# Performance work log

Measured on AMD Instinct MI355X. Metric: run time of the kernel, lower is better.

The kernel has to match this reference:

```python
import jax, jax.numpy as jnp
import numpy as np

N_NODES = 100000
N_EDGES = 1600000
IN_DIM = 128
HID = 128


def setup_inputs() -> dict:
    key = jax.random.key(0)
    ks = jax.random.split(key, 8)
    x = jax.random.normal(ks[0], (N_NODES, IN_DIM), dtype=jnp.float32)
    edge_index = jax.random.randint(ks[1], (2, N_EDGES), 0, N_NODES, dtype=jnp.int32)
    s = 1.0 / np.sqrt(IN_DIM)
    # layer 1: in_dim -> hidden; layer 2: hidden -> hidden
    Wl1 = jax.random.uniform(ks[2], (IN_DIM, HID), jnp.float32, -s, s)
    bl1 = jnp.zeros((HID,), jnp.float32)
    Wr1 = jax.random.uniform(ks[3], (IN_DIM, HID), jnp.float32, -s, s)
    s2 = 1.0 / np.sqrt(HID)
    Wl2 = jax.random.uniform(ks[4], (HID, HID), jnp.float32, -s2, s2)
    bl2 = jnp.zeros((HID,), jnp.float32)
    Wr2 = jax.random.uniform(ks[5], (HID, HID), jnp.float32, -s2, s2)
    return {"x": x, "edge_index": edge_index, "Wl1": Wl1, "bl1": bl1, "Wr1": Wr1,
            "Wl2": Wl2, "bl2": bl2, "Wr2": Wr2}


def _sage_conv(h, src, dst, Wl, bl, Wr, n_nodes):
    # mean aggregation of neighbor (source) features at destination nodes
    msg = h[src]                                               # [E, D] gather
    agg = jax.ops.segment_sum(msg, dst, num_segments=n_nodes)  # [N, D]
    deg = jax.ops.segment_sum(jnp.ones((src.shape[0],), h.dtype), dst,
                              num_segments=n_nodes)            # [N]
    agg = agg / jnp.maximum(deg, 1.0)[:, None]
    # PyG SAGEConv: lin_l(aggregated) + lin_r(root); lin_r has no bias
    return agg @ Wl + bl + h @ Wr


def reference(x, edge_index, Wl1, bl1, Wr1, Wl2, bl2, Wr2):
    src, dst = edge_index[0], edge_index[1]
    n = x.shape[0]
    h = jax.nn.relu(_sage_conv(x, src, dst, Wl1, bl1, Wr1, n))
    # dropout is identity in eval mode
    h = jax.nn.relu(_sage_conv(h, src, dst, Wl2, bl2, Wr2, n))
    return h
```

## Files before the change

kernel.cpp:

```cpp
#include <hip/hip_runtime.h>
#include <stdint.h>

#define DIM 128

typedef __attribute__((ext_vector_type(8))) short short8;
typedef __attribute__((ext_vector_type(4))) float floatx4;

__device__ __forceinline__ unsigned short f2bf(float f){
  union { float f; unsigned int i; } c; c.f = f;
  unsigned int u = c.i;
  return (unsigned short)((u + 0x7fffu + ((u >> 16) & 1u)) >> 16);
}
__device__ __forceinline__ float up_lo(unsigned int v){ return __uint_as_float(v << 16); }
__device__ __forceinline__ float up_hi(unsigned int v){ return __uint_as_float(v & 0xffff0000u); }


__global__ __launch_bounds__(256) void k_cast(const float* __restrict__ in,
    unsigned short* __restrict__ out, int n4){
  int i = blockIdx.x * 256 + threadIdx.x;
  int stride = gridDim.x * 256;
  for (; i < n4; i += stride){
    float4 v = ((const float4*)in)[i];
    ushort4 o;
    o.x = f2bf(v.x); o.y = f2bf(v.y); o.z = f2bf(v.z); o.w = f2bf(v.w);
    ((ushort4*)out)[i] = o;
  }
}


__global__ __launch_bounds__(256) void k_hist256(const int* __restrict__ dst, int E,
    int* __restrict__ bktCnt){
  __shared__ int h[256];
  h[threadIdx.x] = 0;
  __syncthreads();
  int i = blockIdx.x * 256 + threadIdx.x;
  int stride = gridDim.x * 256;
  for (; i < E; i += stride) atomicAdd(&h[dst[i] >> 9], 1);
  __syncthreads();
  int v = h[threadIdx.x];
  if (v) atomicAdd(&bktCnt[threadIdx.x], v);
}

__global__ __launch_bounds__(256) void k_scanB(const int* __restrict__ bktCnt,
    int* __restrict__ bktBase, int NB){
  __shared__ int sd[256];
  int t = threadIdx.x;
  int v = (t < NB) ? bktCnt[t] : 0;
  sd[t] = v;
  __syncthreads();
  #pragma unroll
  for (int off = 1; off < 256; off <<= 1){
    int x = (t >= off) ? sd[t - off] : 0;
    __syncthreads();
    sd[t] += x;
    __syncthreads();
  }
  bktBase[t] = sd[t] - v;
}


__global__ __launch_bounds__(256) void k_hist(const int* __restrict__ dst, int E,
                                              int* __restrict__ deg){
  int e = blockIdx.x * 256 + threadIdx.x;
  if (e < E) atomicAdd(&deg[dst[e]], 1);
}

__global__ __launch_bounds__(256) void k_scan1(const int* __restrict__ deg, int N,
    int* __restrict__ out, int* __restrict__ bsum){
  __shared__ int sd[256];
  int t = threadIdx.x;
  int base = blockIdx.x * 1024 + t * 4;
  int v0=0, v1=0, v2=0, v3=0;
  if (base + 3 < N) { int4 q = *(const int4*)(deg + base); v0=q.x; v1=q.y; v2=q.z; v3=q.w; }
  else {
    if (base + 0 < N) v0 = deg[base + 0];
    if (base + 1 < N) v1 = deg[base + 1];
    if (base + 2 < N) v2 = deg[base + 2];
  }
  int s = v0 + v1 + v2 + v3;
  sd[t] = s;
  __syncthreads();
  #pragma unroll
  for (int off = 1; off < 256; off <<= 1){
    int x = (t >= off) ? sd[t - off] : 0;
    __syncthreads();
    sd[t] += x;
    __syncthreads();
  }
  int inc = sd[t];
  int exc = inc - s;
  if (base + 0 < N) out[base + 0] = exc;
  if (base + 1 < N) out[base + 1] = exc + v0;
  if (base + 2 < N) out[base + 2] = exc + v0 + v1;
  if (base + 3 < N) out[base + 3] = exc + v0 + v1 + v2;
  if (t == 255) bsum[blockIdx.x] = inc;
}

__global__ __launch_bounds__(128) void k_scan2(int* __restrict__ bsum, int nb){
  __shared__ int sd[128];
  int t = threadIdx.x;
  int v = (t < nb) ? bsum[t] : 0;
  sd[t] = v;
  __syncthreads();
  #pragma unroll
  for (int off = 1; off < 128; off <<= 1){
    int x = (t >= off) ? sd[t - off] : 0;
    __syncthreads();
    sd[t] += x;
    __syncthreads();
  }
  if (t < nb) bsum[t] = sd[t] - v;
}

__global__ __launch_bounds__(256) void k_scan3(int* __restrict__ rowptr,
    const int* __restrict__ bsum, int N, int E, int* __restrict__ cursor){
  int i = blockIdx.x * 256 + threadIdx.x;
  if (i < N){
    int v = rowptr[i] + bsum[i >> 10];
    rowptr[i] = v;
    cursor[i] = v;
  }
  if (i == 0) rowptr[N] = E;
}

__global__ __launch_bounds__(256) void k_fill(const int* __restrict__ src,
    const int* __restrict__ dst, int E, int* __restrict__ cursor, int* __restrict__ col){
  int e = blockIdx.x * 256 + threadIdx.x;
  if (e < E){
    int d = dst[e];
    int pos = atomicAdd(&cursor[d], 1);
    col[pos] = src[e];
  }
}


__global__ __launch_bounds__(256) void k_bin(const int* __restrict__ src,
    const int* __restrict__ dst, int E,
    const int* __restrict__ bucketBase, int* __restrict__ cursor,
    int2* __restrict__ binned, int NB){
  __shared__ int2 buf[4096];
  __shared__ unsigned char bidArr[4096];
  __shared__ int cnt[256], startA[256], gstart[256], gbase[256];
  int t = threadIdx.x;
  cnt[t] = 0;
  if (t < NB) gbase[t] = bucketBase[t];
  __syncthreads();
  int base = blockIdx.x * 4096;
  int s_[16], d_[16], r_[16];
  #pragma unroll
  for (int i = 0; i < 16; ++i){
    int e = base + i * 256 + t;
    bool v = (e < E);
    s_[i] = v ? src[e] : 0;
    d_[i] = v ? dst[e] : -1;
    r_[i] = v ? atomicAdd(&cnt[d_[i] >> 9], 1) : 0;
  }
  __syncthreads();
  int v = cnt[t];
  startA[t] = v;
  __syncthreads();
  #pragma unroll
  for (int off = 1; off < 256; off <<= 1){
    int y = (t >= off) ? startA[t - off] : 0;
    __syncthreads();
    startA[t] += y;
    __syncthreads();
  }
  int incl = startA[t];
  __syncthreads();
  startA[t] = incl - v;
  __syncthreads();
  #pragma unroll
  for (int i = 0; i < 16; ++i){
    if (d_[i] >= 0){
      int b = d_[i] >> 9;
      int slot = startA[b] + r_[i];
      buf[slot] = make_int2(s_[i], d_[i]);
      bidArr[slot] = (unsigned char)b;
    }
  }
  if (cnt[t] > 0) gstart[t] = atomicAdd(&cursor[t], cnt[t]);
  __syncthreads();
  int total = startA[255] + cnt[255];
  for (int j = t; j < total; j += 256){
    int b = bidArr[j];
    binned[gbase[b] + gstart[b] + (j - startA[b])] = buf[j];
  }
}


__global__ __launch_bounds__(256) void k_csr2(const int2* __restrict__ binned,
    const int* __restrict__ bktBase, int N, int* __restrict__ rowptr,
    int* __restrict__ col){
  __shared__ int cnt[512], excl[512], cur[512];
  __shared__ int sd[256];
  int b = blockIdx.x;
  int node0 = b << 9;
  int nNodes = min(512, N - node0);
  int t = threadIdx.x;
  cnt[t] = 0; cnt[t + 256] = 0;
  __syncthreads();
  int lo = bktBase[b], hi = bktBase[b + 1];
  for (int e = lo + t; e < hi; e += 256)
    atomicAdd(&cnt[binned[e].y - node0], 1);
  __syncthreads();
  int c0 = cnt[2 * t], c1 = cnt[2 * t + 1];
  int ps = c0 + c1;
  sd[t] = ps;
  __syncthreads();
  #pragma unroll
  for (int off = 1; off < 256; off <<= 1){
    int x = (t >= off) ? sd[t - off] : 0;
    __syncthreads();
    sd[t] += x;
    __syncthreads();
  }
  int pexcl = sd[t] - ps;
  excl[2 * t] = pexcl;
  excl[2 * t + 1] = pexcl + c0;
  cur[2 * t] = 0; cur[2 * t + 1] = 0;
  __syncthreads();
  for (int j = t; j < nNodes; j += 256) rowptr[node0 + j] = lo + excl[j];
  if (t == 0) rowptr[node0 + nNodes] = hi;
  for (int e = lo + t; e < hi; e += 256){
    int2 pr = binned[e];
    int dl = pr.y - node0;
    int loc = atomicAdd(&cur[dl], 1);
    col[lo + excl[dl] + loc] = pr.x;
  }
}


__device__ __forceinline__ void acc8(float* a, uint4 u){
  a[0] += up_lo(u.x); a[1] += up_hi(u.x);
  a[2] += up_lo(u.y); a[3] += up_hi(u.y);
  a[4] += up_lo(u.z); a[5] += up_hi(u.z);
  a[6] += up_lo(u.w); a[7] += up_hi(u.w);
}

__global__ __launch_bounds__(256) void k_agg_bf(const unsigned short* __restrict__ feat,
    const int* __restrict__ rowptr, const int* __restrict__ col,
    unsigned short* __restrict__ out, int N){
  int wid = (blockIdx.x * 256 + threadIdx.x) >> 6;
  if (wid >= N) return;
  int lane = threadIdx.x & 63;
  int q = lane >> 4, s = lane & 15;
  int beg = rowptr[wid], end = rowptr[wid + 1];
  float a[8];
  #pragma unroll
  for (int i = 0; i < 8; ++i) a[i] = 0.f;
  int e = beg;
  for (; e + 16 <= end; e += 16){
    int n0 = col[e + q], n1 = col[e + 4 + q], n2 = col[e + 8 + q], n3 = col[e + 12 + q];
    uint4 u0 = ((const uint4*)(feat + (size_t)n0 * DIM))[s];
    uint4 u1 = ((const uint4*)(feat + (size_t)n1 * DIM))[s];
    uint4 u2 = ((const uint4*)(feat + (size_t)n2 * DIM))[s];
    uint4 u3 = ((const uint4*)(feat + (size_t)n3 * DIM))[s];
    acc8(a, u0); acc8(a, u1); acc8(a, u2); acc8(a, u3);
  }
  for (; e < end; e += 4){
    bool valid = (e + q) < end;
    int idx = valid ? (e + q) : beg;
    int nb = col[idx];
    uint4 u = ((const uint4*)(feat + (size_t)nb * DIM))[s];
    if (valid) acc8(a, u);
  }
  #pragma unroll
  for (int i = 0; i < 8; ++i){
    a[i] += __shfl_xor(a[i], 16, 64);
    a[i] += __shfl_xor(a[i], 32, 64);
  }
  if (q == 0){
    int d = end - beg;
    float r = 1.0f / (float)(d > 1 ? d : 1);
    uint4 o;
    o.x = (unsigned int)f2bf(a[0] * r) | ((unsigned int)f2bf(a[1] * r) << 16);
    o.y = (unsigned int)f2bf(a[2] * r) | ((unsigned int)f2bf(a[3] * r) << 16);
    o.z = (unsigned int)f2bf(a[4] * r) | ((unsigned int)f2bf(a[5] * r) << 16);
    o.w = (unsigned int)f2bf(a[6] * r) | ((unsigned int)f2bf(a[7] * r) << 16);
    ((uint4*)(out + (size_t)wid * DIM))[s] = o;
  }
}


__global__ __launch_bounds__(256) void k_agg_f32(const float* __restrict__ feat,
    const int* __restrict__ rowptr, const int* __restrict__ col,
    unsigned short* __restrict__ out, int N){
  int wid = (blockIdx.x * 256 + threadIdx.x) >> 6;
  if (wid >= N) return;
  int lane = threadIdx.x & 63;
  int beg = rowptr[wid], end = rowptr[wid + 1];
  float a0 = 0.f, a1 = 0.f;
  int off = lane * 2;
  int e = beg;
  for (; e + 4 <= end; e += 4){
    int s0 = col[e], s1 = col[e+1], s2 = col[e+2], s3 = col[e+3];
    float2 v0 = *(const float2*)(feat + (size_t)s0 * DIM + off);
    float2 v1 = *(const float2*)(feat + (size_t)s1 * DIM + off);
    float2 v2 = *(const float2*)(feat + (size_t)s2 * DIM + off);
    float2 v3 = *(const float2*)(feat + (size_t)s3 * DIM + off);
    a0 += v0.x + v1.x + v2.x + v3.x;
    a1 += v0.y + v1.y + v2.y + v3.y;
  }
  for (; e < end; ++e){
    float2 v = *(const float2*)(feat + (size_t)col[e] * DIM + off);
    a0 += v.x; a1 += v.y;
  }
  int d = end - beg;
  float r = 1.0f / (float)(d > 1 ? d : 1);
  a0 *= r; a1 *= r;
  unsigned int o = (unsigned int)f2bf(a0) | ((unsigned int)f2bf(a1) << 16);
  *(unsigned int*)(out + (size_t)wid * DIM + off) = o;
}


template<bool OUTBF>
__global__ __launch_bounds__(256) void k_gemm_r(const unsigned short* __restrict__ A1,
    const unsigned short* __restrict__ A2,
    const float* __restrict__ Wl, const float* __restrict__ Wr,
    const float* __restrict__ bias,
    float* __restrict__ outf, unsigned short* __restrict__ outb, int M)
{
  int lane = threadIdx.x & 63;
  int c = lane & 15, quad = lane >> 4;
  int gwid = blockIdx.x * 4 + (threadIdx.x >> 6);
  int nwaves = gridDim.x * 4;
  int half = gwid & 1;
  int colbase = half * 64;

  short8 B[2][4][4];
  #pragma unroll
  for (int w = 0; w < 2; ++w){
    const float* W = w ? Wr : Wl;
    #pragma unroll
    for (int km = 0; km < 4; ++km){
      #pragma unroll
      for (int j = 0; j < 4; ++j){
        union { short8 v; unsigned short u[8]; } tb;
        #pragma unroll
        for (int i = 0; i < 8; ++i)
          tb.u[i] = f2bf(W[(km * 32 + quad * 8 + i) * 128 + colbase + j * 16 + c]);
        B[w][km][j] = tb.v;
      }
    }
  }
  float bv[4];
  #pragma unroll
  for (int j = 0; j < 4; ++j) bv[j] = bias[colbase + j * 16 + c];

  int ntasks = M >> 4;
  for (int task = gwid >> 1; task < ntasks; task += nwaves >> 1){
    int row0 = task << 4;
    const unsigned short* ap1 = A1 + (size_t)(row0 + c) * DIM + quad * 8;
    const unsigned short* ap2 = A2 + (size_t)(row0 + c) * DIM + quad * 8;
    short8 a1[4], a2[4];
    #pragma unroll
    for (int km = 0; km < 4; ++km){
      a1[km] = *(const short8*)(ap1 + km * 32);
      a2[km] = *(const short8*)(ap2 + km * 32);
    }
    floatx4 acc[4];
    #pragma unroll
    for (int j = 0; j < 4; ++j) acc[j] = (floatx4){0.f, 0.f, 0.f, 0.f};
    #pragma unroll
    for (int km = 0; km < 4; ++km){
      #pragma unroll
      for (int j = 0; j < 4; ++j){
        acc[j] = __builtin_amdgcn_mfma_f32_16x16x32_bf16(a1[km], B[0][km][j], acc[j], 0, 0, 0);
        acc[j] = __builtin_amdgcn_mfma_f32_16x16x32_bf16(a2[km], B[1][km][j], acc[j], 0, 0, 0);
      }
    }
    #pragma unroll
    for (int j = 0; j < 4; ++j){
      int colIdx = colbase + j * 16 + c;
      #pragma unroll
      for (int r = 0; r < 4; ++r){
        int row = row0 + quad * 4 + r;
        float v = fmaxf(acc[j][r] + bv[j], 0.f);
        if (OUTBF) outb[(size_t)row * DIM + colIdx] = f2bf(v);
        else       outf[(size_t)row * DIM + colIdx] = v;
      }
    }
  }
}


__global__ __launch_bounds__(256) void k_gemm_f(const unsigned short* __restrict__ A1,
    const float* __restrict__ A2f,
    const float* __restrict__ Wl, const float* __restrict__ Wr,
    const float* __restrict__ bias, float* __restrict__ outf, int M)
{
  __shared__ unsigned short lds[2 * 128 * 128];
  for (int h = threadIdx.x; h < 128 * 128; h += 256){
    int k = h >> 7, n = h & 127;
    int idx = n * 128 + ((((k >> 3) ^ (n & 7)) << 3)) + (k & 7);
    lds[idx]         = f2bf(Wl[h]);
    lds[16384 + idx] = f2bf(Wr[h]);
  }
  __syncthreads();
  int lane = threadIdx.x & 63;
  int c = lane & 15, quad = lane >> 4;
  int gwid = blockIdx.x * 4 + (threadIdx.x >> 6);
  int nwaves = gridDim.x * 4;
  int ntasks = M >> 4;
  for (int task = gwid; task < ntasks; task += nwaves){
    int row0 = task << 4;
    floatx4 acc[8];
    #pragma unroll
    for (int j = 0; j < 8; ++j) acc[j] = (floatx4){0.f, 0.f, 0.f, 0.f};
    const unsigned short* ap1 = A1 + (size_t)(row0 + c) * DIM + quad * 8;
    #pragma unroll
    for (int km = 0; km < 4; ++km){
      short8 a = *(const short8*)(ap1 + km * 32);
      int kb = (km << 2) + quad;
      #pragma unroll
      for (int j = 0; j < 8; ++j){
        short8 b = *(const short8*)(&lds[(j * 16 + c) * 128 + ((kb ^ (c & 7)) << 3)]);
        acc[j] = __builtin_amdgcn_mfma_f32_16x16x32_bf16(a, b, acc[j], 0, 0, 0);
      }
    }
    #pragma unroll
    for (int km = 0; km < 4; ++km){
      const float* ap2 = A2f + (size_t)(row0 + c) * DIM + quad * 8;
      float4 p0 = *(const float4*)(ap2 + km * 32);
      float4 p1 = *(const float4*)(ap2 + km * 32 + 4);
      union { short8 v; unsigned short u[8]; } ua;
      ua.u[0] = f2bf(p0.x); ua.u[1] = f2bf(p0.y);
      ua.u[2] = f2bf(p0.z); ua.u[3] = f2bf(p0.w);
      ua.u[4] = f2bf(p1.x); ua.u[5] = f2bf(p1.y);
      ua.u[6] = f2bf(p1.z); ua.u[7] = f2bf(p1.w);
      int kb = (km << 2) + quad;
      #pragma unroll
      for (int j = 0; j < 8; ++j){
        short8 b = *(const short8*)(&lds[16384 + (j * 16 + c) * 128 + ((kb ^ (c & 7)) << 3)]);
        acc[j] = __builtin_amdgcn_mfma_f32_16x16x32_bf16(ua.v, b, acc[j], 0, 0, 0);
      }
    }
    #pragma unroll
    for (int j = 0; j < 8; ++j){
      int colIdx = j * 16 + c;
      float bvv = bias[colIdx];
      #pragma unroll
      for (int r = 0; r < 4; ++r){
        int row = row0 + quad * 4 + r;
        outf[(size_t)row * DIM + colIdx] = fmaxf(acc[j][r] + bvv, 0.f);
      }
    }
  }
}


extern "C" void kernel_launch(void* const* d_in, const int* in_sizes, int n_in,
                              void* d_out, int out_size, void* d_ws, size_t ws_size,
                              hipStream_t stream)
{
  const float* x   = (const float*)d_in[0];
  const int*   ei  = (const int*)d_in[1];
  const float* Wl1 = (const float*)d_in[2];
  const float* bl1 = (const float*)d_in[3];
  const float* Wr1 = (const float*)d_in[4];
  const float* Wl2 = (const float*)d_in[5];
  const float* bl2 = (const float*)d_in[6];
  const float* Wr2 = (const float*)d_in[7];

  const int N = in_sizes[0] / DIM;
  const int E = in_sizes[1] / 2;
  const int* src  = ei;
  const int* dstI = ei + E;
  const int NB = (N + 511) >> 9;

  char* p = (char*)d_ws;
  auto alloc = [&](size_t bytes) -> char* {
    char* r = p; p += (bytes + 255) & ~((size_t)255); return r;
  };
  int* rowptr   = (int*)alloc((size_t)(N + 1) * 4);
  int* deg      = (int*)alloc((size_t)N * 4);
  int* bsum     = (int*)alloc(1024);
  int* bktCnt   = (int*)alloc(1024);
  int* bktBase  = (int*)alloc(2048);
  int* bktCur   = (int*)alloc(1024);
  int* col      = (int*)alloc((size_t)E * 4);
  unsigned short* aggb = (unsigned short*)alloc((size_t)N * DIM * 2);
  unsigned short* xb   = (unsigned short*)alloc((size_t)N * DIM * 2);
  unsigned short* h1b  = (unsigned short*)alloc((size_t)N * DIM * 2);
  size_t need_big = (size_t)(p - (char*)d_ws);
  const bool big = (ws_size >= need_big) && (NB <= 255);
  int2* binned = (int2*)aggb;

  int gE = (E + 255) / 256;
  int gAgg = (N * 64 + 255) / 256;

  if (big){
    hipMemsetAsync(bktCnt, 0, 1024, stream);
    hipMemsetAsync(bktCur, 0, 1024, stream);
    k_hist256<<<1024, 256, 0, stream>>>(dstI, E, bktCnt);
    k_scanB<<<1, 256, 0, stream>>>(bktCnt, bktBase, NB);
    k_bin<<<(E + 4095) / 4096, 256, 0, stream>>>(src, dstI, E, bktBase, bktCur,
                                                 binned, NB);
    k_csr2<<<NB, 256, 0, stream>>>(binned, bktBase, N, rowptr, col);
    int n4 = N * DIM / 4;
    k_cast<<<8192, 256, 0, stream>>>(x, xb, n4);
    k_agg_bf<<<gAgg, 256, 0, stream>>>(xb, rowptr, col, aggb, N);
    k_gemm_r<true><<<512, 256, 0, stream>>>(aggb, xb, Wl1, Wr1, bl1,
                                            nullptr, h1b, N);
    k_agg_bf<<<gAgg, 256, 0, stream>>>(h1b, rowptr, col, aggb, N);
    k_gemm_r<false><<<512, 256, 0, stream>>>(aggb, h1b, Wl2, Wr2, bl2,
                                             (float*)d_out, nullptr, N);
  } else {
    hipMemsetAsync(deg, 0, (size_t)N * 4, stream);
    k_hist<<<gE, 256, 0, stream>>>(dstI, E, deg);
    int nb = (N + 1023) / 1024;
    k_scan1<<<nb, 256, 0, stream>>>(deg, N, rowptr, bsum);
    k_scan2<<<1, 128, 0, stream>>>(bsum, nb);
    k_scan3<<<(N + 255) / 256, 256, 0, stream>>>(rowptr, bsum, N, E, deg);
    k_fill<<<gE, 256, 0, stream>>>(src, dstI, E, deg, col);
    float* h1 = (float*)d_out;
    k_agg_f32<<<gAgg, 256, 0, stream>>>(x, rowptr, col, aggb, N);
    k_gemm_f<<<512, 256, 0, stream>>>(aggb, x, Wl1, Wr1, bl1, h1, N);
    k_agg_f32<<<gAgg, 256, 0, stream>>>(h1, rowptr, col, aggb, N);
    k_gemm_f<<<512, 256, 0, stream>>>(aggb, h1, Wl2, Wr2, bl2, (float*)d_out, N);
  }
}
```

Before: 347.6 us.

## Fuse neighbor aggregation with SAGE GEMM into one persistent kernel per layer

Replaces the separate bf16 aggregation kernel and MFMA GEMM kernel with one fused kernel per layer. Each 128-thread block handles a 16-row tile. It stages column indices in LDS, gathers and averages neighbor features per row, writes the bf16 aggregate to LDS, then runs the MFMA against register-resident weights. This removes the aggregate buffer's global write and read and one launch per layer. In exchange, work per lane now follows the maximum degree within each 16-row tile, so divergence rises, and each block reloads and converts the weights once.

After: 356.5 us. +2.6%, slower.

```diff
diff --git a/kernel.cpp b/kernel.cpp
--- a/kernel.cpp
+++ b/kernel.cpp
@@ -231,6 +231,8 @@
 }
 
 
+#define CAP 1024
+
 __device__ __forceinline__ void acc8(float* a, uint4 u){
   a[0] += up_lo(u.x); a[1] += up_hi(u.x);
   a[2] += up_lo(u.y); a[3] += up_hi(u.y);
@@ -238,47 +240,142 @@
   a[6] += up_lo(u.w); a[7] += up_hi(u.w);
 }
 
-__global__ __launch_bounds__(256) void k_agg_bf(const unsigned short* __restrict__ feat,
+template<bool OUTBF>
+__global__ __launch_bounds__(128, 2) void k_fused(const unsigned short* __restrict__ feat,
     const int* __restrict__ rowptr, const int* __restrict__ col,
-    unsigned short* __restrict__ out, int N){
-  int wid = (blockIdx.x * 256 + threadIdx.x) >> 6;
-  if (wid >= N) return;
+    const float* __restrict__ Wl, const float* __restrict__ Wr,
+    const float* __restrict__ bias,
+    float* __restrict__ outf, unsigned short* __restrict__ outb, int N)
+{
+  __shared__ int lds_col[CAP];
+  __shared__ __align__(16) unsigned short lds_a[16 * 136];
+
   int lane = threadIdx.x & 63;
-  int q = lane >> 4, s = lane & 15;
-  int beg = rowptr[wid], end = rowptr[wid + 1];
-  float a[8];
-  #pragma unroll
-  for (int i = 0; i < 8; ++i) a[i] = 0.f;
-  int e = beg;
-  for (; e + 16 <= end; e += 16){
-    int n0 = col[e + q], n1 = col[e + 4 + q], n2 = col[e + 8 + q], n3 = col[e + 12 + q];
-    uint4 u0 = ((const uint4*)(feat + (size_t)n0 * DIM))[s];
-    uint4 u1 = ((const uint4*)(feat + (size_t)n1 * DIM))[s];
-    uint4 u2 = ((const uint4*)(feat + (size_t)n2 * DIM))[s];
-    uint4 u3 = ((const uint4*)(feat + (size_t)n3 * DIM))[s];
-    acc8(a, u0); acc8(a, u1); acc8(a, u2); acc8(a, u3);
-  }
-  for (; e < end; e += 4){
-    bool valid = (e + q) < end;
-    int idx = valid ? (e + q) : beg;
-    int nb = col[idx];
-    uint4 u = ((const uint4*)(feat + (size_t)nb * DIM))[s];
-    if (valid) acc8(a, u);
-  }
-  #pragma unroll
-  for (int i = 0; i < 8; ++i){
-    a[i] += __shfl_xor(a[i], 16, 64);
-    a[i] += __shfl_xor(a[i], 32, 64);
-  }
-  if (q == 0){
-    int d = end - beg;
-    float r = 1.0f / (float)(d > 1 ? d : 1);
-    uint4 o;
-    o.x = (unsigned int)f2bf(a[0] * r) | ((unsigned int)f2bf(a[1] * r) << 16);
-    o.y = (unsigned int)f2bf(a[2] * r) | ((unsigned int)f2bf(a[3] * r) << 16);
-    o.z = (unsigned int)f2bf(a[4] * r) | ((unsigned int)f2bf(a[5] * r) << 16);
-    o.w = (unsigned int)f2bf(a[6] * r) | ((unsigned int)f2bf(a[7] * r) << 16);
-    ((uint4*)(out + (size_t)wid * DIM))[s] = o;
+  int c = lane & 15, q = lane >> 4;
+  int h = threadIdx.x >> 6;
+  int colbase = h * 64;
+
+  short8 B[2][4][4];
+  #pragma unroll
+  for (int w = 0; w < 2; ++w){
+    const float* W = w ? Wr : Wl;
+    #pragma unroll
+    for (int km = 0; km < 4; ++km){
+      #pragma unroll
+      for (int j = 0; j < 4; ++j){
+        union { short8 v; unsigned short u[8]; } tb;
+        #pragma unroll
+        for (int i = 0; i < 8; ++i)
+          tb.u[i] = f2bf(W[(km * 32 + q * 8 + i) * 128 + colbase + j * 16 + c]);
+        B[w][km][j] = tb.v;
+      }
+    }
+  }
+  float bv[4];
+  #pragma unroll
+  for (int j = 0; j < 4; ++j) bv[j] = bias[colbase + j * 16 + c];
+
+  int ntiles = (N + 15) >> 4;
+  for (int task = blockIdx.x; task < ntiles; task += gridDim.x){
+    int row0 = task << 4;
+    int myrow = row0 + c;
+    int rb = myrow < N ? myrow : N;
+    int re = (myrow + 1) < N ? (myrow + 1) : N;
+    int beg = rowptr[rb];
+    int end = rowptr[re];
+    if (myrow >= N) end = beg;
+    int deg = end - beg;
+    int lo = __shfl(beg, 0, 64);
+    int hi = __shfl(end, 15, 64);
+
+    float a0[8], a1v[8];
+    #pragma unroll
+    for (int i = 0; i < 8; ++i){ a0[i] = 0.f; a1v[i] = 0.f; }
+
+    for (int base = lo; base < hi; base += CAP){
+      int len = hi - base; if (len > CAP) len = CAP;
+      __syncthreads();
+      for (int j2 = threadIdx.x; j2 < len; j2 += 128) lds_col[j2] = col[base + j2];
+      __syncthreads();
+      int klo = beg > base ? beg : base;
+      int khi = end < base + CAP ? end : base + CAP;
+      int cnt = khi - klo; if (cnt < 0) cnt = 0;
+      int off = klo - base;
+      int mx = cnt;
+      #pragma unroll
+      for (int d = 1; d < 16; d <<= 1) mx = max(mx, __shfl_xor(mx, d, 64));
+
+      int fofs = h * 64 + q * 8;
+      for (int kb = 0; kb < mx; kb += 4){
+        int k0 = off + kb, k1 = k0 + 1, k2 = k0 + 2, k3 = k0 + 3;
+        int i0 = lds_col[k0 < CAP ? k0 : 0];
+        int i1 = lds_col[k1 < CAP ? k1 : 0];
+        int i2 = lds_col[k2 < CAP ? k2 : 0];
+        int i3 = lds_col[k3 < CAP ? k3 : 0];
+        bool v0 = kb + 0 < cnt, v1 = kb + 1 < cnt, v2 = kb + 2 < cnt, v3 = kb + 3 < cnt;
+        if (!v0) i0 = 0;
+        if (!v1) i1 = 0;
+        if (!v2) i2 = 0;
+        if (!v3) i3 = 0;
+        const unsigned short* f0 = feat + (size_t)i0 * DIM + fofs;
+        const unsigned short* f1 = feat + (size_t)i1 * DIM + fofs;
+        const unsigned short* f2 = feat + (size_t)i2 * DIM + fofs;
+        const unsigned short* f3 = feat + (size_t)i3 * DIM + fofs;
+        uint4 u00 = *(const uint4*)f0;        uint4 u01 = *(const uint4*)(f0 + 32);
+        uint4 u10 = *(const uint4*)f1;        uint4 u11 = *(const uint4*)(f1 + 32);
+        uint4 u20 = *(const uint4*)f2;        uint4 u21 = *(const uint4*)(f2 + 32);
+        uint4 u30 = *(const uint4*)f3;        uint4 u31 = *(const uint4*)(f3 + 32);
+        if (v0){ acc8(a0, u00); acc8(a1v, u01); }
+        if (v1){ acc8(a0, u10); acc8(a1v, u11); }
+        if (v2){ acc8(a0, u20); acc8(a1v, u21); }
+        if (v3){ acc8(a0, u30); acc8(a1v, u31); }
+      }
+    }
+
+    float r = 1.0f / (float)(deg > 1 ? deg : 1);
+    union { short8 v; unsigned short u[8]; } pa, pb;
+    #pragma unroll
+    for (int i = 0; i < 8; ++i){ pa.u[i] = f2bf(a0[i] * r); pb.u[i] = f2bf(a1v[i] * r); }
+    int la = c * 136 + h * 64 + q * 8;
+    *(short8*)&lds_a[la]      = pa.v;
+    *(short8*)&lds_a[la + 32] = pb.v;
+
+    int rowA = myrow < N ? myrow : (N - 1);
+    const unsigned short* ap2 = feat + (size_t)rowA * DIM + q * 8;
+    short8 a2[4];
+    #pragma unroll
+    for (int km = 0; km < 4; ++km) a2[km] = *(const short8*)(ap2 + km * 32);
+
+    __syncthreads();
+    short8 a1[4];
+    #pragma unroll
+    for (int km = 0; km < 4; ++km)
+      a1[km] = *(const short8*)&lds_a[c * 136 + km * 32 + q * 8];
+
+    floatx4 acc[4];
+    #pragma unroll
+    for (int j = 0; j < 4; ++j) acc[j] = (floatx4){0.f, 0.f, 0.f, 0.f};
+    #pragma unroll
+    for (int km = 0; km < 4; ++km){
+      #pragma unroll
+      for (int j = 0; j < 4; ++j){
+        acc[j] = __builtin_amdgcn_mfma_f32_16x16x32_bf16(a1[km], B[0][km][j], acc[j], 0, 0, 0);
+        acc[j] = __builtin_amdgcn_mfma_f32_16x16x32_bf16(a2[km], B[1][km][j], acc[j], 0, 0, 0);
+      }
+    }
+    #pragma unroll
+    for (int j = 0; j < 4; ++j){
+      int colIdx = colbase + j * 16 + c;
+      #pragma unroll
+      for (int rr = 0; rr < 4; ++rr){
+        int row = row0 + q * 4 + rr;
+        if (row < N){
+          float v = fmaxf(acc[j][rr] + bv[j], 0.f);
+          if (OUTBF) outb[(size_t)row * DIM + colIdx] = f2bf(v);
+          else       outf[(size_t)row * DIM + colIdx] = v;
+        }
+      }
+    }
   }
 }
 
@@ -314,77 +411,6 @@
 }
 
 
-template<bool OUTBF>
-__global__ __launch_bounds__(256) void k_gemm_r(const unsigned short* __restrict__ A1,
-    const unsigned short* __restrict__ A2,
-    const float* __restrict__ Wl, const float* __restrict__ Wr,
-    const float* __restrict__ bias,
-    float* __restrict__ outf, unsigned short* __restrict__ outb, int M)
-{
-  int lane = threadIdx.x & 63;
-  int c = lane & 15, quad = lane >> 4;
-  int gwid = blockIdx.x * 4 + (threadIdx.x >> 6);
-  int nwaves = gridDim.x * 4;
-  int half = gwid & 1;
-  int colbase = half * 64;
-
-  short8 B[2][4][4];
-  #pragma unroll
-  for (int w = 0; w < 2; ++w){
-    const float* W = w ? Wr : Wl;
-    #pragma unroll
-    for (int km = 0; km < 4; ++km){
-      #pragma unroll
-      for (int j = 0; j < 4; ++j){
-        union { short8 v; unsigned short u[8]; } tb;
-        #pragma unroll
-        for (int i = 0; i < 8; ++i)
-          tb.u[i] = f2bf(W[(km * 32 + quad * 8 + i) * 128 + colbase + j * 16 + c]);
-        B[w][km][j] = tb.v;
-      }
-    }
-  }
-  float bv[4];
-  #pragma unroll
-  for (int j = 0; j < 4; ++j) bv[j] = bias[colbase + j * 16 + c];
-
-  int ntasks = M >> 4;
-  for (int task = gwid >> 1; task < ntasks; task += nwaves >> 1){
-    int row0 = task << 4;
-    const unsigned short* ap1 = A1 + (size_t)(row0 + c) * DIM + quad * 8;
-    const unsigned short* ap2 = A2 + (size_t)(row0 + c) * DIM + quad * 8;
-    short8 a1[4], a2[4];
-    #pragma unroll
-    for (int km = 0; km < 4; ++km){
-      a1[km] = *(const short8*)(ap1 + km * 32);
-      a2[km] = *(const short8*)(ap2 + km * 32);
-    }
-    floatx4 acc[4];
-    #pragma unroll
-    for (int j = 0; j < 4; ++j) acc[j] = (floatx4){0.f, 0.f, 0.f, 0.f};
-    #pragma unroll
-    for (int km = 0; km < 4; ++km){
-      #pragma unroll
-      for (int j = 0; j < 4; ++j){
-        acc[j] = __builtin_amdgcn_mfma_f32_16x16x32_bf16(a1[km], B[0][km][j], acc[j], 0, 0, 0);
-        acc[j] = __builtin_amdgcn_mfma_f32_16x16x32_bf16(a2[km], B[1][km][j], acc[j], 0, 0, 0);
-      }
-    }
-    #pragma unroll
-    for (int j = 0; j < 4; ++j){
-      int colIdx = colbase + j * 16 + c;
-      #pragma unroll
-      for (int r = 0; r < 4; ++r){
-        int row = row0 + quad * 4 + r;
-        float v = fmaxf(acc[j][r] + bv[j], 0.f);
-        if (OUTBF) outb[(size_t)row * DIM + colIdx] = f2bf(v);
-        else       outf[(size_t)row * DIM + colIdx] = v;
-      }
-    }
-  }
-}
-
-
 __global__ __launch_bounds__(256) void k_gemm_f(const unsigned short* __restrict__ A1,
     const float* __restrict__ A2f,
     const float* __restrict__ Wl, const float* __restrict__ Wr,
@@ -500,11 +526,9 @@
     k_csr2<<<NB, 256, 0, stream>>>(binned, bktBase, N, rowptr, col);
     int n4 = N * DIM / 4;
     k_cast<<<8192, 256, 0, stream>>>(x, xb, n4);
-    k_agg_bf<<<gAgg, 256, 0, stream>>>(xb, rowptr, col, aggb, N);
-    k_gemm_r<true><<<512, 256, 0, stream>>>(aggb, xb, Wl1, Wr1, bl1,
+    k_fused<true><<<1024, 128, 0, stream>>>(xb, rowptr, col, Wl1, Wr1, bl1,
                                             nullptr, h1b, N);
-    k_agg_bf<<<gAgg, 256, 0, stream>>>(h1b, rowptr, col, aggb, N);
-    k_gemm_r<false><<<512, 256, 0, stream>>>(aggb, h1b, Wl2, Wr2, bl2,
+    k_fused<false><<<1024, 128, 0, stream>>>(h1b, rowptr, col, Wl2, Wr2, bl2,
                                              (float*)d_out, nullptr, N);
   } else {
     hipMemsetAsync(deg, 0, (size_t)N * 4, stream);
```

## Fuse cast with histogram, merge memsets, rework bf16 aggregation gather

Applied to the files above, without the earlier changes.

The fp32-to-bf16 cast of x is merged into the dst-bucket histogram kernel. bktCur is moved next to bktCnt so one memset clears both, removing a launch and a memset. The bf16 aggregation now has each lane read one 4-byte pair per neighbor, with 16 neighbor indices broadcast via readlane. This replaces 16-byte-per-lane loads over 4 neighbor groups and the cross-lane shuffle reduction. The cost is narrower loads and more load instructions per edge, while rows are still read as whole 256-byte contiguous segments.

Measured after the change: 422.4 us. 21.5% more time.

```diff
diff --git a/kernel.cpp b/kernel.cpp
--- a/kernel.cpp
+++ b/kernel.cpp
@@ -15,27 +15,21 @@
 __device__ __forceinline__ float up_hi(unsigned int v){ return __uint_as_float(v & 0xffff0000u); }
 
 
-__global__ __launch_bounds__(256) void k_cast(const float* __restrict__ in,
-    unsigned short* __restrict__ out, int n4){
+__global__ __launch_bounds__(256) void k_prep(const float* __restrict__ in,
+    unsigned short* __restrict__ out, int n4,
+    const int* __restrict__ dst, int E, int* __restrict__ bktCnt){
+  __shared__ int h[256];
+  h[threadIdx.x] = 0;
+  __syncthreads();
   int i = blockIdx.x * 256 + threadIdx.x;
   int stride = gridDim.x * 256;
-  for (; i < n4; i += stride){
-    float4 v = ((const float4*)in)[i];
+  for (int k = i; k < n4; k += stride){
+    float4 v = ((const float4*)in)[k];
     ushort4 o;
     o.x = f2bf(v.x); o.y = f2bf(v.y); o.z = f2bf(v.z); o.w = f2bf(v.w);
-    ((ushort4*)out)[i] = o;
-  }
-}
-
-
-__global__ __launch_bounds__(256) void k_hist256(const int* __restrict__ dst, int E,
-    int* __restrict__ bktCnt){
-  __shared__ int h[256];
-  h[threadIdx.x] = 0;
-  __syncthreads();
-  int i = blockIdx.x * 256 + threadIdx.x;
-  int stride = gridDim.x * 256;
-  for (; i < E; i += stride) atomicAdd(&h[dst[i] >> 9], 1);
+    ((ushort4*)out)[k] = o;
+  }
+  for (int k = i; k < E; k += stride) atomicAdd(&h[dst[k] >> 9], 1);
   __syncthreads();
   int v = h[threadIdx.x];
   if (v) atomicAdd(&bktCnt[threadIdx.x], v);
@@ -231,55 +225,38 @@
 }
 
 
-__device__ __forceinline__ void acc8(float* a, uint4 u){
-  a[0] += up_lo(u.x); a[1] += up_hi(u.x);
-  a[2] += up_lo(u.y); a[3] += up_hi(u.y);
-  a[4] += up_lo(u.z); a[5] += up_hi(u.z);
-  a[6] += up_lo(u.w); a[7] += up_hi(u.w);
-}
-
 __global__ __launch_bounds__(256) void k_agg_bf(const unsigned short* __restrict__ feat,
     const int* __restrict__ rowptr, const int* __restrict__ col,
     unsigned short* __restrict__ out, int N){
   int wid = (blockIdx.x * 256 + threadIdx.x) >> 6;
   if (wid >= N) return;
   int lane = threadIdx.x & 63;
-  int q = lane >> 4, s = lane & 15;
-  int beg = rowptr[wid], end = rowptr[wid + 1];
-  float a[8];
-  #pragma unroll
-  for (int i = 0; i < 8; ++i) a[i] = 0.f;
-  int e = beg;
-  for (; e + 16 <= end; e += 16){
-    int n0 = col[e + q], n1 = col[e + 4 + q], n2 = col[e + 8 + q], n3 = col[e + 12 + q];
-    uint4 u0 = ((const uint4*)(feat + (size_t)n0 * DIM))[s];
-    uint4 u1 = ((const uint4*)(feat + (size_t)n1 * DIM))[s];
-    uint4 u2 = ((const uint4*)(feat + (size_t)n2 * DIM))[s];
-    uint4 u3 = ((const uint4*)(feat + (size_t)n3 * DIM))[s];
-    acc8(a, u0); acc8(a, u1); acc8(a, u2); acc8(a, u3);
-  }
-  for (; e < end; e += 4){
-    bool valid = (e + q) < end;
-    int idx = valid ? (e + q) : beg;
-    int nb = col[idx];
-    uint4 u = ((const uint4*)(feat + (size_t)nb * DIM))[s];
-    if (valid) acc8(a, u);
-  }
-  #pragma unroll
-  for (int i = 0; i < 8; ++i){
-    a[i] += __shfl_xor(a[i], 16, 64);
-    a[i] += __shfl_xor(a[i], 32, 64);
-  }
-  if (q == 0){
-    int d = end - beg;
-    float r = 1.0f / (float)(d > 1 ? d : 1);
-    uint4 o;
-    o.x = (unsigned int)f2bf(a[0] * r) | ((unsigned int)f2bf(a[1] * r) << 16);
-    o.y = (unsigned int)f2bf(a[2] * r) | ((unsigned int)f2bf(a[3] * r) << 16);
-    o.z = (unsigned int)f2bf(a[4] * r) | ((unsigned int)f2bf(a[5] * r) << 16);
-    o.w = (unsigned int)f2bf(a[6] * r) | ((unsigned int)f2bf(a[7] * r) << 16);
-    ((uint4*)(out + (size_t)wid * DIM))[s] = o;
-  }
+  int beg = __builtin_amdgcn_readfirstlane(rowptr[wid]);
+  int end = __builtin_amdgcn_readfirstlane(rowptr[wid + 1]);
+  int deg = end - beg;
+  float a0 = 0.f, a1 = 0.f;
+  int ls = lane & 15;
+
+  for (int e = beg; e < end; e += 16){
+    int cnt = end - e; cnt = cnt > 16 ? 16 : cnt;
+    int idx = col[e + (ls < cnt ? ls : 0)];
+    unsigned int u[16];
+    #pragma unroll
+    for (int j = 0; j < 16; ++j){
+      if (j < cnt){
+        int n = __builtin_amdgcn_readlane(idx, j);
+        u[j] = *(const unsigned int*)(feat + (size_t)n * DIM + (lane << 1));
+      }
+    }
+    #pragma unroll
+    for (int j = 0; j < 16; ++j){
+      if (j < cnt){ a0 += up_lo(u[j]); a1 += up_hi(u[j]); }
+    }
+  }
+
+  float r = 1.0f / (float)(deg > 1 ? deg : 1);
+  unsigned int o = (unsigned int)f2bf(a0 * r) | ((unsigned int)f2bf(a1 * r) << 16);
+  *(unsigned int*)(out + (size_t)wid * DIM + (lane << 1)) = o;
 }
 
 
@@ -477,8 +454,8 @@
   int* deg      = (int*)alloc((size_t)N * 4);
   int* bsum     = (int*)alloc(1024);
   int* bktCnt   = (int*)alloc(1024);
+  int* bktCur   = (int*)alloc(1024);
   int* bktBase  = (int*)alloc(2048);
-  int* bktCur   = (int*)alloc(1024);
   int* col      = (int*)alloc((size_t)E * 4);
   unsigned short* aggb = (unsigned short*)alloc((size_t)N * DIM * 2);
   unsigned short* xb   = (unsigned short*)alloc((size_t)N * DIM * 2);
@@ -491,15 +468,13 @@
   int gAgg = (N * 64 + 255) / 256;
 
   if (big){
-    hipMemsetAsync(bktCnt, 0, 1024, stream);
-    hipMemsetAsync(bktCur, 0, 1024, stream);
-    k_hist256<<<1024, 256, 0, stream>>>(dstI, E, bktCnt);
+    int n4 = N * DIM / 4;
+    hipMemsetAsync(bktCnt, 0, 2048, stream);
+    k_prep<<<1024, 256, 0, stream>>>(x, xb, n4, dstI, E, bktCnt);
     k_scanB<<<1, 256, 0, stream>>>(bktCnt, bktBase, NB);
     k_bin<<<(E + 4095) / 4096, 256, 0, stream>>>(src, dstI, E, bktBase, bktCur,
                                                  binned, NB);
     k_csr2<<<NB, 256, 0, stream>>>(binned, bktBase, N, rowptr, col);
-    int n4 = N * DIM / 4;
-    k_cast<<<8192, 256, 0, stream>>>(x, xb, n4);
     k_agg_bf<<<gAgg, 256, 0, stream>>>(xb, rowptr, col, aggb, N);
     k_gemm_r<true><<<512, 256, 0, stream>>>(aggb, xb, Wl1, Wr1, bl1,
                                             nullptr, h1b, N);
```
